# Kernel tuning notes

Measured on AMD Instinct MI355X. Metric: run time of the kernel, lower is better.

Reference implementation:

```python
import jax, jax.numpy as jnp
import numpy as np

N_NODES = 50000
N_FEAT = 512
N_HID = 128
N_CLASS = 8
N_EDGES = 640000


def setup_inputs() -> dict:
    key = jax.random.key(0)
    k1, k2, k3, k4, k5 = jax.random.split(key, 5)
    x = jax.random.normal(k1, (N_NODES, N_FEAT), dtype=jnp.float32)
    edge_index = jax.random.randint(k2, (2, N_EDGES), 0, N_NODES, dtype=jnp.int64)
    # GCNConv linear weight (glorot), stored as [nfeat, nhid] for x @ W
    s_conv = jnp.sqrt(6.0 / (N_FEAT + N_HID)).astype(jnp.float32)
    W_conv = jax.random.uniform(k3, (N_FEAT, N_HID), jnp.float32, -s_conv, s_conv)
    b_conv = jnp.zeros((N_HID,), jnp.float32)
    # fc head, xavier_uniform per weights_init, bias zero
    s_fc = jnp.sqrt(6.0 / (N_HID + N_CLASS)).astype(jnp.float32)
    W_fc = jax.random.uniform(k4, (N_HID, N_CLASS), jnp.float32, -s_fc, s_fc)
    b_fc = jnp.zeros((N_CLASS,), jnp.float32)
    return {"x": x, "edge_index": edge_index, "W_conv": W_conv,
            "b_conv": b_conv, "W_fc": W_fc, "b_fc": b_fc}


def reference(x, edge_index, W_conv, b_conv, W_fc, b_fc):
    N = x.shape[0]
    # GCNConv: add self-loops, symmetric normalization deg^-1/2 A deg^-1/2
    loop = jnp.arange(N, dtype=edge_index.dtype)
    src = jnp.concatenate([edge_index[0], loop])  # [E+N]
    dst = jnp.concatenate([edge_index[1], loop])
    ones = jnp.ones(src.shape[0], dtype=x.dtype)
    deg = jax.ops.segment_sum(ones, dst, num_segments=N)  # in-degree incl. self loop
    dinv = jnp.where(deg > 0, jax.lax.rsqrt(deg), 0.0)
    norm = dinv[src] * dinv[dst]  # [E+N]
    h = x @ W_conv  # [N, nhid] dense transform before propagation
    msg = h[src] * norm[:, None]  # gather + scale, [E+N, nhid]
    out = jax.ops.segment_sum(msg, dst, num_segments=N) + b_conv  # scatter-add
    # linear classification head
    return out @ W_fc + b_fc  # [N, nclass]
```

## Files before the change

kernel.cpp:

```cpp
#include <hip/hip_runtime.h>
#include <hip/hip_bf16.h>

#define NFEAT 512
#define NCLS 8
#define NHID 128
#define CAP 64
#define NTILES 3125

typedef float4 f4;
typedef unsigned short u16;
typedef short bf16x8 __attribute__((ext_vector_type(8)));
typedef float f32x4 __attribute__((ext_vector_type(4)));

__device__ inline u16 f2bf(float f) {
    __hip_bfloat16 h = __float2bfloat16(f);
    u16 u;
    __builtin_memcpy(&u, &h, 2);
    return u;
}

__global__ __launch_bounds__(256) void init_kernel(
    const float* __restrict__ W1, const float* __restrict__ W2,
    const float* __restrict__ b1, const float* __restrict__ b2,
    u16* __restrict__ WbT, float* __restrict__ bias2,
    int* __restrict__ cursor, int N)
{
    int t = blockIdx.x * 256 + threadIdx.x;
    if (t < N) cursor[t] = 0;
    if (t < NFEAT * NCLS) {
        int k = t >> 3, c = t & 7;
        const float* w1r = W1 + k * NHID;
        float acc = 0.f;
        #pragma unroll 8
        for (int j = 0; j < NHID; ++j) acc = fmaf(w1r[j], W2[j * NCLS + c], acc);
        WbT[c * NFEAT + k] = f2bf(acc);
        WbT[(c + 8) * NFEAT + k] = 0;
    }
    if (t < NCLS) {
        float acc = b2[t];
        for (int j = 0; j < NHID; ++j) acc = fmaf(b1[j], W2[j * NCLS + t], acc);
        bias2[t] = acc;
    }
}

__global__ __launch_bounds__(256) void fused_kernel(
    const int* __restrict__ src, const int* __restrict__ dst,
    const float* __restrict__ x, const u16* __restrict__ WbT,
    int* __restrict__ cursor, u16* __restrict__ eidx,
    float* __restrict__ g, int N, int E)
{
    const int tid  = threadIdx.x;
    const int bid  = blockIdx.x;
    const int lane = tid & 63;
    const int wid  = bid * 4 + (tid >> 6);
    const int r16  = lane & 15;
    const int g4   = lane >> 4;

    auto do_edges = [&]() {
        int e = bid * 256 + tid;
        if (e < E) {
            int d = dst[e];
            int pos = atomicAdd(&cursor[d], 1);
            if (pos < CAP) eidx[(size_t)d * CAP + pos] = (u16)src[e];
        }
    };

    auto do_gemm = [&]() {
        if (wid >= NTILES) return;
        const int row0 = wid * 16;
        const float* xr = x + (size_t)(row0 + r16) * NFEAT + g4 * 8;
        const u16*   wp = WbT + r16 * NFEAT + g4 * 8;
        f32x4 acc = {0.f, 0.f, 0.f, 0.f};
        #pragma unroll
        for (int ks = 0; ks < NFEAT / 32; ++ks) {
            f4 p = *(const f4*)(xr + ks * 32);
            f4 q = *(const f4*)(xr + ks * 32 + 4);
            union { bf16x8 v; u16 u[8]; } af;
            af.u[0] = f2bf(p.x); af.u[1] = f2bf(p.y);
            af.u[2] = f2bf(p.z); af.u[3] = f2bf(p.w);
            af.u[4] = f2bf(q.x); af.u[5] = f2bf(q.y);
            af.u[6] = f2bf(q.z); af.u[7] = f2bf(q.w);
            bf16x8 bv = *(const bf16x8*)(wp + ks * 32);
            acc = __builtin_amdgcn_mfma_f32_16x16x32_bf16(af.v, bv, acc, 0, 0, 0);
        }
        if (r16 < NCLS) {
            #pragma unroll
            for (int r = 0; r < 4; ++r)
                g[(size_t)(row0 + g4 * 4 + r) * 8 + r16] = acc[r];
        }
    };

    if (bid & 1) { do_edges(); do_gemm(); }
    else         { do_gemm(); do_edges(); }
}

__global__ __launch_bounds__(256) void gather_kernel(
    const int* __restrict__ cursor, const u16* __restrict__ eidx,
    const float* __restrict__ g, const float* __restrict__ bias2,
    float* __restrict__ out, int N)
{
    int t = blockIdx.x * 256 + threadIdx.x;
    int i = t >> 3, c = t & 7;
    if (i >= N) return;
    int n = min(cursor[i], CAP);
    const u16* slot = eidx + (size_t)i * CAP;
    float acc = 0.f;
    for (int k = 0; k < n; ++k) {
        int s = slot[k];
        float ds = rsqrtf((float)cursor[s] + 1.0f);
        acc = fmaf(g[(size_t)s * 8 + c], ds, acc);
    }
    float di = rsqrtf((float)cursor[i] + 1.0f);
    out[t] = fmaf(di, acc + di * g[(size_t)i * 8 + c], bias2[c]);
}

extern "C" void kernel_launch(void* const* d_in, const int* in_sizes, int n_in,
                              void* d_out, int out_size, void* d_ws, size_t ws_size,
                              hipStream_t stream)
{
    const float* x  = (const float*)d_in[0];
    const int*   ei = (const int*)d_in[1];
    const float* W1 = (const float*)d_in[2];
    const float* b1 = (const float*)d_in[3];
    const float* W2 = (const float*)d_in[4];
    const float* b2 = (const float*)d_in[5];
    float* out = (float*)d_out;

    const int N = in_sizes[0] / NFEAT;
    const int E = in_sizes[1] / 2;
    const int* src = ei;
    const int* dst = ei + E;

    char* ws = (char*)d_ws;
    size_t off = 0;
    auto alloc = [&](size_t bytes) {
        char* p = ws + off;
        off += (bytes + 255) & ~(size_t)255;
        return p;
    };
    int*   cursor = (int*)alloc((size_t)N * 4);
    u16*   eidx   = (u16*)alloc((size_t)N * CAP * 2);
    float* g      = (float*)alloc((size_t)N * 8 * 4);
    u16*   WbT    = (u16*)alloc((size_t)16 * NFEAT * 2);
    float* bias2  = (float*)alloc(NCLS * 4);

    const int NB = (N + 255) / 256;
    const int FB = (E + 255) / 256;

    init_kernel<<<NB, 256, 0, stream>>>(W1, W2, b1, b2, WbT, bias2, cursor, N);

    fused_kernel<<<FB, 256, 0, stream>>>(src, dst, x, WbT, cursor, eidx, g, N, E);

    gather_kernel<<<(N * 8 + 255) / 256, 256, 0, stream>>>(cursor, eidx, g, bias2, out, N);
}
```

Before: 69.04 us.

## Replace global-atomic edge bucketing with two-pass binned counting sort

Edges are bucketed by 16-node destination bins using per-window shared-memory histograms, a column prefix scan, and a second scatter pass into fixed-capacity bin buffers. Degree scaling is applied to g in a separate pass, and the gather accumulates per-bin in shared memory with LDS atomics. The aim is to remove contended global atomics and scattered per-node slot writes. In exchange it adds more kernel launches and extra passes over the edge list.

```diff
diff --git a/kernel.cpp b/kernel.cpp
--- a/kernel.cpp
+++ b/kernel.cpp
@@ -4,29 +4,33 @@
 #define NFEAT 512
 #define NCLS 8
 #define NHID 128
-#define CAP 64
+#define NPB 16
+#define NBIN 3125
+#define NBIN16 3136
+#define NBG 196
+#define WINE 1024
+#define NW 625
+#define BINCAP 320
 #define NTILES 3125
 
 typedef float4 f4;
 typedef unsigned short u16;
+typedef unsigned int u32;
 typedef short bf16x8 __attribute__((ext_vector_type(8)));
 typedef float f32x4 __attribute__((ext_vector_type(4)));
 
 __device__ inline u16 f2bf(float f) {
     __hip_bfloat16 h = __float2bfloat16(f);
-    u16 u;
-    __builtin_memcpy(&u, &h, 2);
+    u16 u; __builtin_memcpy(&u, &h, 2);
     return u;
 }
 
 __global__ __launch_bounds__(256) void init_kernel(
     const float* __restrict__ W1, const float* __restrict__ W2,
     const float* __restrict__ b1, const float* __restrict__ b2,
-    u16* __restrict__ WbT, float* __restrict__ bias2,
-    int* __restrict__ cursor, int N)
+    u16* __restrict__ WbT, float* __restrict__ bias2)
 {
     int t = blockIdx.x * 256 + threadIdx.x;
-    if (t < N) cursor[t] = 0;
     if (t < NFEAT * NCLS) {
         int k = t >> 3, c = t & 7;
         const float* w1r = W1 + k * NHID;
@@ -43,10 +47,9 @@
     }
 }
 
-__global__ __launch_bounds__(256) void fused_kernel(
-    const int* __restrict__ src, const int* __restrict__ dst,
-    const float* __restrict__ x, const u16* __restrict__ WbT,
-    int* __restrict__ cursor, u16* __restrict__ eidx,
+__global__ __launch_bounds__(256) void histgemm_kernel(
+    const int* __restrict__ dst, const float* __restrict__ x,
+    const u16* __restrict__ WbT, int* __restrict__ wincnt,
     float* __restrict__ g, int N, int E)
 {
     const int tid  = threadIdx.x;
@@ -56,12 +59,23 @@
     const int r16  = lane & 15;
     const int g4   = lane >> 4;
 
-    auto do_edges = [&]() {
-        int e = bid * 256 + tid;
-        if (e < E) {
-            int d = dst[e];
-            int pos = atomicAdd(&cursor[d], 1);
-            if (pos < CAP) eidx[(size_t)d * CAP + pos] = (u16)src[e];
+    __shared__ int hist[NBIN16];
+
+    auto do_hist = [&]() {
+        if (bid >= NW) return;
+        for (int k = tid; k < NBIN16; k += 256) hist[k] = 0;
+        __syncthreads();
+        int e0 = bid * WINE;
+        #pragma unroll
+        for (int j = 0; j < 4; ++j) {
+            int e = e0 + j * 256 + tid;
+            if (e < E) atomicAdd(&hist[dst[e] >> 4], 1);
+        }
+        __syncthreads();
+        if (tid < NBG) {
+            int4* d4 = (int4*)(wincnt + (size_t)tid * NW * 16 + (size_t)bid * 16);
+            const int4* s4 = (const int4*)(hist + tid * 16);
+            d4[0] = s4[0]; d4[1] = s4[1]; d4[2] = s4[2]; d4[3] = s4[3];
         }
     };
 
@@ -90,28 +104,129 @@
         }
     };
 
-    if (bid & 1) { do_edges(); do_gemm(); }
-    else         { do_gemm(); do_edges(); }
+    if (bid & 1) { do_hist(); do_gemm(); }
+    else         { do_gemm(); do_hist(); }
+}
+
+__global__ __launch_bounds__(256) void colprefix_kernel(
+    int* __restrict__ wincnt, int* __restrict__ colsum)
+{
+    const int bg = blockIdx.x;
+    const int t = threadIdx.x;
+    const int bl = t & 15, chunk = t >> 4;
+    const int CPW = (NW + 15) / 16;
+    int vals[40];
+    int s = 0;
+    for (int k = 0; k < CPW; ++k) {
+        int win = chunk * CPW + k;
+        int v = (win < NW) ? wincnt[(size_t)bg * NW * 16 + (size_t)win * 16 + bl] : 0;
+        vals[k] = v; s += v;
+    }
+    __shared__ int part[256];
+    part[bl * 16 + chunk] = s;
+    __syncthreads();
+    int base = 0;
+    for (int c = 0; c < chunk; ++c) base += part[bl * 16 + c];
+    int run = base;
+    for (int k = 0; k < CPW; ++k) {
+        int win = chunk * CPW + k;
+        if (win < NW) {
+            wincnt[(size_t)bg * NW * 16 + (size_t)win * 16 + bl] = run;
+            run += vals[k];
+        }
+    }
+    if (chunk == 15) colsum[bg * 16 + bl] = run;
+}
+
+__global__ __launch_bounds__(256) void pass2_kernel(
+    const int* __restrict__ src, const int* __restrict__ dst,
+    const int* __restrict__ wincnt, u32* __restrict__ ebuf, int E)
+{
+    const int w = blockIdx.x;
+    const int tid = threadIdx.x;
+    __shared__ int loff[NBIN16];
+    __shared__ int rank[NBIN16];
+    for (int k = tid; k < NBIN16; k += 256) {
+        loff[k] = wincnt[(size_t)(k >> 4) * NW * 16 + (size_t)w * 16 + (k & 15)];
+        rank[k] = 0;
+    }
+    __syncthreads();
+    int e0 = w * WINE;
+    #pragma unroll
+    for (int j = 0; j < 4; ++j) {
+        int e = e0 + j * 256 + tid;
+        if (e < E) {
+            int d = dst[e];
+            int b = d >> 4;
+            int r = atomicAdd(&rank[b], 1);
+            int pos = loff[b] + r;
+            if (pos < BINCAP) {
+                u32 val = (u32)src[e] | ((u32)(d & 15) << 16);
+                __builtin_nontemporal_store(val, &ebuf[(size_t)b * BINCAP + pos]);
+            }
+        }
+    }
+}
+
+__global__ __launch_bounds__(256) void degscale_kernel(
+    const u32* __restrict__ ebuf, const int* __restrict__ colsum,
+    float* __restrict__ g, int* __restrict__ deg)
+{
+    const int tid = threadIdx.x;
+    const int wv = tid >> 6, lane = tid & 63;
+    const int bin = blockIdx.x * 4 + wv;
+    if (bin >= NBIN) return;
+    __shared__ int cnt_s[4][NPB];
+    if (lane < NPB) cnt_s[wv][lane] = 0;
+    int cnt = min(colsum[bin], BINCAP);
+    const u32* eb = ebuf + (size_t)bin * BINCAP;
+    for (int k = lane; k < cnt; k += 64)
+        atomicAdd(&cnt_s[wv][eb[k] >> 16], 1);
+    #pragma unroll
+    for (int half = 0; half < 2; ++half) {
+        int k2 = lane + half * 64;
+        int node = k2 >> 3, c = k2 & 7;
+        int i = bin * NPB + node;
+        float di = rsqrtf((float)cnt_s[wv][node] + 1.0f);
+        g[(size_t)i * 8 + c] *= di;
+    }
+    if (lane < NPB) deg[bin * NPB + lane] = cnt_s[wv][lane];
 }
 
 __global__ __launch_bounds__(256) void gather_kernel(
-    const int* __restrict__ cursor, const u16* __restrict__ eidx,
-    const float* __restrict__ g, const float* __restrict__ bias2,
-    float* __restrict__ out, int N)
-{
-    int t = blockIdx.x * 256 + threadIdx.x;
-    int i = t >> 3, c = t & 7;
-    if (i >= N) return;
-    int n = min(cursor[i], CAP);
-    const u16* slot = eidx + (size_t)i * CAP;
-    float acc = 0.f;
-    for (int k = 0; k < n; ++k) {
-        int s = slot[k];
-        float ds = rsqrtf((float)cursor[s] + 1.0f);
-        acc = fmaf(g[(size_t)s * 8 + c], ds, acc);
-    }
-    float di = rsqrtf((float)cursor[i] + 1.0f);
-    out[t] = fmaf(di, acc + di * g[(size_t)i * 8 + c], bias2[c]);
+    const u32* __restrict__ ebuf, const int* __restrict__ colsum,
+    const float* __restrict__ g, const int* __restrict__ deg,
+    const float* __restrict__ bias2, float* __restrict__ out)
+{
+    const int tid = threadIdx.x;
+    const int wv = tid >> 6, lane = tid & 63;
+    const int bin = blockIdx.x * 4 + wv;
+    if (bin >= NBIN) return;
+    __shared__ float acc_s[4][NPB * 8];
+    acc_s[wv][lane] = 0.f;
+    acc_s[wv][lane + 64] = 0.f;
+    int cnt = min(colsum[bin], BINCAP);
+    const u32* eb = ebuf + (size_t)bin * BINCAP;
+    for (int k = lane; k < cnt; k += 64) {
+        u32 u = eb[k];
+        int s = u & 0xFFFF;
+        int dl = u >> 16;
+        const f4* gs = (const f4*)(g + (size_t)s * 8);
+        f4 a = gs[0], b = gs[1];
+        float* A = &acc_s[wv][dl * 8];
+        atomicAdd(A + 0, a.x); atomicAdd(A + 1, a.y);
+        atomicAdd(A + 2, a.z); atomicAdd(A + 3, a.w);
+        atomicAdd(A + 4, b.x); atomicAdd(A + 5, b.y);
+        atomicAdd(A + 6, b.z); atomicAdd(A + 7, b.w);
+    }
+    #pragma unroll
+    for (int half = 0; half < 2; ++half) {
+        int k2 = lane + half * 64;
+        int node = k2 >> 3, c = k2 & 7;
+        int i = bin * NPB + node;
+        float di = rsqrtf((float)deg[i] + 1.0f);
+        out[(size_t)i * 8 + c] = fmaf(di, acc_s[wv][k2] + g[(size_t)i * 8 + c], bias2[c]);
+    }
 }
 
 extern "C" void kernel_launch(void* const* d_in, const int* in_sizes, int n_in,
@@ -138,18 +253,26 @@
         off += (bytes + 255) & ~(size_t)255;
         return p;
     };
-    int*   cursor = (int*)alloc((size_t)N * 4);
-    u16*   eidx   = (u16*)alloc((size_t)N * CAP * 2);
+    int*   wincnt = (int*)alloc((size_t)NBG * NW * 16 * 4);
+    int*   colsum = (int*)alloc((size_t)NBIN16 * 4);
+    u32*   ebuf   = (u32*)alloc((size_t)NBIN * BINCAP * 4);
     float* g      = (float*)alloc((size_t)N * 8 * 4);
+    int*   deg    = (int*)alloc((size_t)N * 4);
     u16*   WbT    = (u16*)alloc((size_t)16 * NFEAT * 2);
     float* bias2  = (float*)alloc(NCLS * 4);
 
-    const int NB = (N + 255) / 256;
-    const int FB = (E + 255) / 256;
-
-    init_kernel<<<NB, 256, 0, stream>>>(W1, W2, b1, b2, WbT, bias2, cursor, N);
-
-    fused_kernel<<<FB, 256, 0, stream>>>(src, dst, x, WbT, cursor, eidx, g, N, E);
-
-    gather_kernel<<<(N * 8 + 255) / 256, 256, 0, stream>>>(cursor, eidx, g, bias2, out, N);
-}
+    const int FB = 782;
+    const int BB = (NBIN + 3) / 4;
+
+    init_kernel<<<(NFEAT * NCLS + 255) / 256, 256, 0, stream>>>(W1, W2, b1, b2, WbT, bias2);
+
+    histgemm_kernel<<<FB, 256, 0, stream>>>(dst, x, WbT, wincnt, g, N, E);
+
+    colprefix_kernel<<<NBG, 256, 0, stream>>>(wincnt, colsum);
+
+    pass2_kernel<<<NW, 256, 0, stream>>>(src, dst, wincnt, ebuf, E);
+
+    degscale_kernel<<<BB, 256, 0, stream>>>(ebuf, colsum, g, deg);
+
+    gather_kernel<<<BB, 256, 0, stream>>>(ebuf, colsum, g, deg, bias2, out);
+}
```

After: 110.4 us. 1.6x slower.
